# Kernel tuning notes

Measured on AMD Instinct MI355X. Metric: run time of the kernel, lower is better.

The kernel has to match this reference:

```python
import jax, jax.numpy as jnp
import numpy as np

B, C_IN, C_OUT, H, W = 16, 64, 64, 192, 192
K_DY, KS, STRIDE, PAD = 4, 3, 1, 1
TEMP = 30.0
HID = int(C_IN * 0.25) + 1  # 17, matches hidden_channels rule for in_channels != 3
GROUPS = 8
EPS = 1e-5
NEG_SLOPE = 0.01


def setup_inputs() -> dict:
    key = jax.random.key(0)
    ks = jax.random.split(key, 6)
    return {
        "x": jax.random.normal(ks[0], (B, C_IN, H, W), jnp.float32),
        "attn_w1": jax.random.normal(ks[1], (HID, C_IN), jnp.float32) * 0.1,   # 1x1 conv, no bias
        "attn_w2": jax.random.normal(ks[2], (K_DY, HID), jnp.float32) * 0.1,   # 1x1 conv
        "attn_b2": jnp.zeros((K_DY,), jnp.float32),
        "weights": jax.random.normal(ks[3], (K_DY, C_OUT, C_IN, KS, KS), jnp.float32),
        "gn_gamma": jnp.ones((C_OUT,), jnp.float32),
        "gn_beta": jnp.zeros((C_OUT,), jnp.float32),
    }


def reference(x, attn_w1, attn_w2, attn_b2, weights, gn_gamma, gn_beta):
    b = x.shape[0]
    # SE-style attention over the dynamic-filter bank
    pooled = x.mean(axis=(2, 3))                       # (b, c_in) global avg pool
    h = jax.nn.relu(pooled @ attn_w1.T)                # (b, hid)
    scores = h @ attn_w2.T + attn_b2                   # (b, K)
    attn = jax.nn.softmax(scores / TEMP, axis=1)       # (b, K)
    # Per-sample synthesized filters
    filters = jnp.einsum('bk,koihw->boihw', attn, weights)   # (b, out_c, in_c, kh, kw)
    filters = filters.reshape(b * C_OUT, C_IN, KS, KS)
    # Grouped conv: groups = batch, each sample convolved with its own filter
    xg = x.reshape(1, b * C_IN, H, W)
    y = jax.lax.conv_general_dilated(
        xg, filters,
        window_strides=(STRIDE, STRIDE),
        padding=[(PAD, PAD), (PAD, PAD)],
        dimension_numbers=('NCHW', 'OIHW', 'NCHW'),
        feature_group_count=b,
    )
    y = y.reshape(b, C_OUT, y.shape[2], y.shape[3])
    # GroupNorm(8 groups) + LeakyReLU
    yg = y.reshape(b, GROUPS, C_OUT // GROUPS, y.shape[2], y.shape[3])
    mean = yg.mean(axis=(2, 3, 4), keepdims=True)
    var = yg.var(axis=(2, 3, 4), keepdims=True)
    yn = ((yg - mean) * jax.lax.rsqrt(var + EPS)).reshape(y.shape)
    yn = yn * gn_gamma[None, :, None, None] + gn_beta[None, :, None, None]
    return jnp.where(yn >= 0, yn, NEG_SLOPE * yn)
```

## Files before the change

kernel.cpp:

```cpp
#include <hip/hip_runtime.h>

typedef unsigned short u16;
typedef unsigned int u32;
typedef _Float16 f16;
typedef __attribute__((ext_vector_type(8))) f16 v8h;
typedef __attribute__((ext_vector_type(4))) f16 v4h;
typedef __attribute__((ext_vector_type(16))) float v16f;

#define BN 16
#define CHN 64
#define HH 192
#define WW 192
#define HWSZ 36864
#define KDY 4
#define HIDN 17
#define NG 8
#define TEMP_ 30.0f
#define EPSV 1e-5f
#define NSLOPE 0.01f
#define NTILE 144

#define TR 8
#define TC 32
#define HR 10
#define HC 34
#define PSTR 34

__device__ float g_pp[BN * NTILE * CHN];
__device__ float g_attn[BN * KDY];
__device__ float g_stats[BN * NG * 2];
__device__ __align__(16) f16 g_filt[BN * 9 * CHN * CHN];
__device__ __align__(16) f16 g_xh[(size_t)BN * HWSZ * CHN];

__global__ void __launch_bounds__(256) trans_pool_kernel(const float* __restrict__ x) {
    __shared__ u32 ts[256 * 34];
    const int b = blockIdx.y, tile = blockIdx.x;
    const int t = threadIdx.x;
    const int p0 = tile * 256;
    const float* xb = x + (size_t)b * CHN * HWSZ + p0;
    #pragma unroll 4
    for (int cp = 0; cp < 32; cp++) {
        float v0 = xb[(size_t)(2 * cp) * HWSZ + t];
        float v1 = xb[(size_t)(2 * cp + 1) * HWSZ + t];
        u32 pk = (u32)__builtin_bit_cast(u16, (f16)v0)
               | ((u32)__builtin_bit_cast(u16, (f16)v1) << 16);
        ts[t * 34 + cp] = pk;
    }
    __syncthreads();
    f16* dp = g_xh + ((size_t)b * HWSZ + p0 + t) * CHN;
    const u32* src = ts + t * 34;
    #pragma unroll
    for (int i = 0; i < 8; i++) {
        uint2 a = *(const uint2*)(src + 4 * i);
        uint2 c = *(const uint2*)(src + 4 * i + 2);
        ((uint4*)dp)[i] = make_uint4(a.x, a.y, c.x, c.y);
    }
    const int cp = t & 31, seg = t >> 5;
    float s0 = 0.f, s1 = 0.f;
    for (int p = 0; p < 32; p++) {
        u32 pk = ts[(seg * 32 + p) * 34 + cp];
        s0 += (float)__builtin_bit_cast(f16, (u16)(pk & 0xffffu));
        s1 += (float)__builtin_bit_cast(f16, (u16)(pk >> 16));
    }
    s0 += __shfl_down(s0, 32);
    s1 += __shfl_down(s1, 32);
    __syncthreads();
    float* ps = (float*)ts;
    const int lane = t & 63, w = t >> 6;
    if (lane < 32) { ps[(w * 32 + lane) * 2] = s0; ps[(w * 32 + lane) * 2 + 1] = s1; }
    __syncthreads();
    if (t < 32) {
        float a0 = ps[t * 2] + ps[(32 + t) * 2] + ps[(64 + t) * 2] + ps[(96 + t) * 2];
        float a1 = ps[t * 2 + 1] + ps[(32 + t) * 2 + 1]
                 + ps[(64 + t) * 2 + 1] + ps[(96 + t) * 2 + 1];
        float* gp = g_pp + ((size_t)b * NTILE + tile) * CHN;
        gp[2 * t] = a0; gp[2 * t + 1] = a1;
    }
}

__global__ void attn_kernel(const float* __restrict__ w1, const float* __restrict__ w2,
                            const float* __restrict__ b2) {
    const int b = blockIdx.x, t = threadIdx.x;
    if (t < NG * 2) g_stats[b * NG * 2 + t] = 0.f;
    float s = 0.f;
    const float* gp = g_pp + (size_t)b * NTILE * CHN + t;
    for (int i = 0; i < NTILE; i++) s += gp[i * CHN];
    __shared__ float pr[CHN];
    __shared__ float hs[HIDN];
    pr[t] = s * (1.0f / HWSZ);
    __syncthreads();
    if (t < HIDN) {
        float a = 0.f;
        for (int c = 0; c < CHN; c++) a += w1[t * CHN + c] * pr[c];
        hs[t] = fmaxf(a, 0.f);
    }
    __syncthreads();
    if (t == 0) {
        float scv[KDY]; float m = -3e38f;
        #pragma unroll
        for (int k = 0; k < KDY; k++) {
            float sc = b2[k];
            for (int h = 0; h < HIDN; h++) sc += w2[k * HIDN + h] * hs[h];
            sc *= (1.0f / TEMP_);
            scv[k] = sc; m = fmaxf(m, sc);
        }
        float den = 0.f;
        #pragma unroll
        for (int k = 0; k < KDY; k++) { scv[k] = __expf(scv[k] - m); den += scv[k]; }
        float rd = 1.f / den;
        #pragma unroll
        for (int k = 0; k < KDY; k++) g_attn[b * KDY + k] = scv[k] * rd;
    }
}

__global__ void filt_kernel(const float* __restrict__ wts) {
    __shared__ float at[BN * KDY];
    if (threadIdx.x < BN * KDY) at[threadIdx.x] = g_attn[threadIdx.x];
    __syncthreads();
    int t = blockIdx.x * 256 + threadIdx.x;
    int tap = t / 4096;
    int co = (t >> 6) & 63;
    int ci = t & 63;
    float w0 = wts[((0 * CHN + co) * CHN + ci) * 9 + tap];
    float w1 = wts[((1 * CHN + co) * CHN + ci) * 9 + tap];
    float w2 = wts[((2 * CHN + co) * CHN + ci) * 9 + tap];
    float w3 = wts[((3 * CHN + co) * CHN + ci) * 9 + tap];
    #pragma unroll
    for (int b = 0; b < BN; b++) {
        float v = at[b * 4] * w0 + at[b * 4 + 1] * w1
                + at[b * 4 + 2] * w2 + at[b * 4 + 3] * w3;
        g_filt[((b * 9 + tap) * CHN + co) * CHN + ci] = (f16)v;
    }
}

__global__ void __launch_bounds__(256, 3) conv_kernel(float* __restrict__ y) {
    __shared__ __align__(16) u32 xs[HR * HC * PSTR];
    __shared__ float gsum[NG], gsq[NG];
    const int b = blockIdx.z;
    const int r0 = blockIdx.y * TR, c0 = blockIdx.x * TC;
    const int tid = threadIdx.x;
    const int w = tid >> 6, lane = tid & 63;
    const int n = lane & 31, hi = lane >> 5;
    if (tid < NG) { gsum[tid] = 0.f; gsq[tid] = 0.f; }

    const f16* xhb = g_xh + (size_t)b * HWSZ * CHN;
    for (int l = tid; l < HR * HC * 8; l += 256) {
        int pix = l >> 3, part = l & 7;
        int hr = pix / HC, hc = pix - hr * HC;
        int gr = r0 - 1 + hr, gc = c0 - 1 + hc;
        uint4 v = make_uint4(0, 0, 0, 0);
        if ((unsigned)gr < HH && (unsigned)gc < WW)
            v = *(const uint4*)(xhb + ((size_t)(gr * WW + gc)) * CHN + part * 8);
        u32* d = xs + pix * PSTR + part * 4;
        *(uint2*)d = make_uint2(v.x, v.y);
        *(uint2*)(d + 2) = make_uint2(v.z, v.w);
    }
    __syncthreads();

    const f16* xsh = (const f16*)xs;
    const f16* fb = g_filt + (size_t)b * 9 * CHN * CHN + (size_t)n * CHN + hi * 8;
    v16f acc00 = {}, acc01 = {}, acc10 = {}, acc11 = {};

    v8h A0[4], A1[4];
    #pragma unroll
    for (int kb = 0; kb < 4; kb++) {
        A0[kb] = *(const v8h*)(fb + kb * 16);
        A1[kb] = *(const v8h*)(fb + kb * 16 + 32 * CHN);
    }
    #pragma unroll
    for (int tap = 0; tap < 9; tap++) {
        v8h P0[4], P1[4];
        if (tap < 8) {
            const f16* fp = fb + (tap + 1) * (CHN * CHN);
            #pragma unroll
            for (int kb = 0; kb < 4; kb++) {
                P0[kb] = *(const v8h*)(fp + kb * 16);
                P1[kb] = *(const v8h*)(fp + kb * 16 + 32 * CHN);
            }
        }
        const int dy = tap / 3, dx = tap - 3 * (tap / 3);
        const f16* xr = xsh + ((2 * w + dy) * HC + (n + dx)) * (PSTR * 2) + hi * 8;
        #pragma unroll
        for (int kb = 0; kb < 4; kb++) {
            v4h lo0 = *(const v4h*)(xr + kb * 16);
            v4h up0 = *(const v4h*)(xr + kb * 16 + 4);
            v4h lo1 = *(const v4h*)(xr + kb * 16 + HC * PSTR * 2);
            v4h up1 = *(const v4h*)(xr + kb * 16 + 4 + HC * PSTR * 2);
            v8h b0 = __builtin_shufflevector(lo0, up0, 0, 1, 2, 3, 4, 5, 6, 7);
            v8h b1 = __builtin_shufflevector(lo1, up1, 0, 1, 2, 3, 4, 5, 6, 7);
            acc00 = __builtin_amdgcn_mfma_f32_32x32x16_f16(A0[kb], b0, acc00, 0, 0, 0);
            acc01 = __builtin_amdgcn_mfma_f32_32x32x16_f16(A0[kb], b1, acc01, 0, 0, 0);
            acc10 = __builtin_amdgcn_mfma_f32_32x32x16_f16(A1[kb], b0, acc10, 0, 0, 0);
            acc11 = __builtin_amdgcn_mfma_f32_32x32x16_f16(A1[kb], b1, acc11, 0, 0, 0);
        }
        if (tap < 8) {
            #pragma unroll
            for (int kb = 0; kb < 4; kb++) { A0[kb] = P0[kb]; A1[kb] = P1[kb]; }
        }
    }

    float sg[NG], sq[NG];
    #pragma unroll
    for (int g = 0; g < NG; g++) { sg[g] = 0.f; sq[g] = 0.f; }
    float* yb = y + (size_t)b * CHN * HWSZ + (size_t)(r0 + 2 * w) * WW + (c0 + n);
#define EPI(ACC, CH, J) { v16f a = ACC; \
    _Pragma("unroll") \
    for (int r = 0; r < 16; r++) { \
        int co = CH * 32 + (r & 3) + 8 * (r >> 2) + 4 * hi; \
        yb[(size_t)co * HWSZ + J * WW] = a[r]; \
        int g = (r >> 2) + 4 * CH; \
        sg[g] += a[r]; sq[g] += a[r] * a[r]; } }
    EPI(acc00, 0, 0) EPI(acc01, 0, 1) EPI(acc10, 1, 0) EPI(acc11, 1, 1)
#undef EPI
    #pragma unroll
    for (int g = 0; g < NG; g++) {
        float s = sg[g], q = sq[g];
        #pragma unroll
        for (int off = 32; off > 0; off >>= 1) {
            s += __shfl_down(s, off);
            q += __shfl_down(q, off);
        }
        if (lane == 0) { atomicAdd(&gsum[g], s); atomicAdd(&gsq[g], q); }
    }
    __syncthreads();
    if (tid < 2 * NG) {
        int g = tid >> 1, which = tid & 1;
        atomicAdd(&g_stats[(b * NG + g) * 2 + which], which ? gsq[g] : gsum[g]);
    }
}

__global__ void norm_kernel(float* __restrict__ y, const float* __restrict__ gamma,
                            const float* __restrict__ beta) {
    int i8 = blockIdx.x * 256 + threadIdx.x;
    int idx = i8 * 8;
    int b = idx / (CHN * HWSZ);
    int co = (idx / HWSZ) & (CHN - 1);
    int g = co >> 3;
    const float invN = 1.0f / (8.0f * HWSZ);
    float mean = g_stats[(b * NG + g) * 2 + 0] * invN;
    float var = fmaxf(g_stats[(b * NG + g) * 2 + 1] * invN - mean * mean, 0.f);
    float sc = rsqrtf(var + EPSV) * gamma[co];
    float sh = beta[co] - mean * sc;
    float4* yp = (float4*)y + i8 * 2;
    float4 v0 = yp[0], v1 = yp[1];
    float vv[8] = {v0.x, v0.y, v0.z, v0.w, v1.x, v1.y, v1.z, v1.w};
    #pragma unroll
    for (int t = 0; t < 8; t++) {
        float a = vv[t] * sc + sh;
        vv[t] = a >= 0.f ? a : NSLOPE * a;
    }
    yp[0] = make_float4(vv[0], vv[1], vv[2], vv[3]);
    yp[1] = make_float4(vv[4], vv[5], vv[6], vv[7]);
}

extern "C" void kernel_launch(void* const* d_in, const int* in_sizes, int n_in,
                              void* d_out, int out_size, void* d_ws, size_t ws_size,
                              hipStream_t stream) {
    const float* x     = (const float*)d_in[0];
    const float* w1    = (const float*)d_in[1];
    const float* w2    = (const float*)d_in[2];
    const float* b2    = (const float*)d_in[3];
    const float* wts   = (const float*)d_in[4];
    const float* gamma = (const float*)d_in[5];
    const float* beta  = (const float*)d_in[6];
    float* out = (float*)d_out;

    dim3 tg(NTILE, BN);
    trans_pool_kernel<<<tg, 256, 0, stream>>>(x);
    attn_kernel<<<BN, 64, 0, stream>>>(w1, w2, b2);
    filt_kernel<<<144, 256, 0, stream>>>(wts);
    dim3 cg(WW / TC, HH / TR, BN);
    conv_kernel<<<cg, 256, 0, stream>>>(out);
    norm_kernel<<<BN * CHN * HWSZ / 8 / 256, 256, 0, stream>>>(out, gamma, beta);
}
```

Before: 432.1 us.

## Store conv output as fp16 intermediate, batch halo loads, swizzle blocks, widen attn

The conv kernel now writes its pre-norm output to an fp16 scratch buffer, and the norm kernel reads that buffer before writing the fp32 output. This halves the intermediate write and read traffic, at some precision cost before GroupNorm. The halo load is split into issuing all global loads into registers first and then storing to LDS, which adds memory-level parallelism but uses more registers. Blocks are remapped with an XCD-style swizzle, and the attention pooling reduction now uses 256 threads instead of 64.

After: 406.7 us. 5.9% less time.

```diff
diff --git a/kernel.cpp b/kernel.cpp
--- a/kernel.cpp
+++ b/kernel.cpp
@@ -25,12 +25,14 @@
 #define HR 10
 #define HC 34
 #define PSTR 34
+#define NCHUNK (HR * HC * 8)
 
 __device__ float g_pp[BN * NTILE * CHN];
 __device__ float g_attn[BN * KDY];
 __device__ float g_stats[BN * NG * 2];
 __device__ __align__(16) f16 g_filt[BN * 9 * CHN * CHN];
 __device__ __align__(16) f16 g_xh[(size_t)BN * HWSZ * CHN];
+__device__ __align__(16) f16 g_yh[(size_t)BN * CHN * HWSZ];
 
 __global__ void __launch_bounds__(256) trans_pool_kernel(const float* __restrict__ x) {
     __shared__ u32 ts[256 * 34];
@@ -78,20 +80,27 @@
     }
 }
 
-__global__ void attn_kernel(const float* __restrict__ w1, const float* __restrict__ w2,
-                            const float* __restrict__ b2) {
+__global__ void __launch_bounds__(256) attn_kernel(const float* __restrict__ w1,
+                                                   const float* __restrict__ w2,
+                                                   const float* __restrict__ b2) {
+    __shared__ float red[256];
+    __shared__ float pr[CHN];
+    __shared__ float hs[HIDN];
     const int b = blockIdx.x, t = threadIdx.x;
     if (t < NG * 2) g_stats[b * NG * 2 + t] = 0.f;
+    const int c = t & 63, part = t >> 6;
+    const float* gp = g_pp + (size_t)b * NTILE * CHN + c;
     float s = 0.f;
-    const float* gp = g_pp + (size_t)b * NTILE * CHN + t;
-    for (int i = 0; i < NTILE; i++) s += gp[i * CHN];
-    __shared__ float pr[CHN];
-    __shared__ float hs[HIDN];
-    pr[t] = s * (1.0f / HWSZ);
+    #pragma unroll 4
+    for (int i = part * 36; i < part * 36 + 36; i++) s += gp[i * CHN];
+    red[t] = s;
+    __syncthreads();
+    if (t < CHN)
+        pr[t] = (red[t] + red[t + 64] + red[t + 128] + red[t + 192]) * (1.0f / HWSZ);
     __syncthreads();
     if (t < HIDN) {
         float a = 0.f;
-        for (int c = 0; c < CHN; c++) a += w1[t * CHN + c] * pr[c];
+        for (int cc = 0; cc < CHN; cc++) a += w1[t * CHN + cc] * pr[cc];
         hs[t] = fmaxf(a, 0.f);
     }
     __syncthreads();
@@ -133,27 +142,44 @@
     }
 }
 
-__global__ void __launch_bounds__(256, 3) conv_kernel(float* __restrict__ y) {
+__global__ void __launch_bounds__(256, 3) conv_kernel() {
     __shared__ __align__(16) u32 xs[HR * HC * PSTR];
     __shared__ float gsum[NG], gsq[NG];
-    const int b = blockIdx.z;
-    const int r0 = blockIdx.y * TR, c0 = blockIdx.x * TC;
+    const int bid = blockIdx.x;
+    const int swz = (bid & 7) * 288 + (bid >> 3);
+    const int b = swz / 144;
+    const int rem = swz - b * 144;
+    const int r0 = (rem / 6) * TR, c0 = (rem % 6) * TC;
     const int tid = threadIdx.x;
     const int w = tid >> 6, lane = tid & 63;
     const int n = lane & 31, hi = lane >> 5;
     if (tid < NG) { gsum[tid] = 0.f; gsq[tid] = 0.f; }
 
     const f16* xhb = g_xh + (size_t)b * HWSZ * CHN;
-    for (int l = tid; l < HR * HC * 8; l += 256) {
+    uint4 rv[11];
+    #pragma unroll
+    for (int i = 0; i < 11; i++) {
+        int l = tid + i * 256;
         int pix = l >> 3, part = l & 7;
         int hr = pix / HC, hc = pix - hr * HC;
         int gr = r0 - 1 + hr, gc = c0 - 1 + hc;
-        uint4 v = make_uint4(0, 0, 0, 0);
-        if ((unsigned)gr < HH && (unsigned)gc < WW)
-            v = *(const uint4*)(xhb + ((size_t)(gr * WW + gc)) * CHN + part * 8);
-        u32* d = xs + pix * PSTR + part * 4;
-        *(uint2*)d = make_uint2(v.x, v.y);
-        *(uint2*)(d + 2) = make_uint2(v.z, v.w);
+        bool ok = (l < NCHUNK) && ((unsigned)gr < HH) && ((unsigned)gc < WW);
+        size_t off = ok ? ((size_t)(gr * WW + gc) * CHN + part * 8) : 0;
+        rv[i] = *(const uint4*)(xhb + off);
+    }
+    #pragma unroll
+    for (int i = 0; i < 11; i++) {
+        int l = tid + i * 256;
+        if (l < NCHUNK) {
+            int pix = l >> 3, part = l & 7;
+            int hr = pix / HC, hc = pix - hr * HC;
+            int gr = r0 - 1 + hr, gc = c0 - 1 + hc;
+            bool ok = ((unsigned)gr < HH) && ((unsigned)gc < WW);
+            uint4 v = ok ? rv[i] : make_uint4(0, 0, 0, 0);
+            u32* d = xs + pix * PSTR + part * 4;
+            *(uint2*)d = make_uint2(v.x, v.y);
+            *(uint2*)(d + 2) = make_uint2(v.z, v.w);
+        }
     }
     __syncthreads();
 
@@ -202,12 +228,12 @@
     float sg[NG], sq[NG];
     #pragma unroll
     for (int g = 0; g < NG; g++) { sg[g] = 0.f; sq[g] = 0.f; }
-    float* yb = y + (size_t)b * CHN * HWSZ + (size_t)(r0 + 2 * w) * WW + (c0 + n);
+    f16* yb = g_yh + (size_t)b * CHN * HWSZ + (size_t)(r0 + 2 * w) * WW + (c0 + n);
 #define EPI(ACC, CH, J) { v16f a = ACC; \
     _Pragma("unroll") \
     for (int r = 0; r < 16; r++) { \
         int co = CH * 32 + (r & 3) + 8 * (r >> 2) + 4 * hi; \
-        yb[(size_t)co * HWSZ + J * WW] = a[r]; \
+        yb[(size_t)co * HWSZ + J * WW] = (f16)a[r]; \
         int g = (r >> 2) + 4 * CH; \
         sg[g] += a[r]; sq[g] += a[r] * a[r]; } }
     EPI(acc00, 0, 0) EPI(acc01, 0, 1) EPI(acc10, 1, 0) EPI(acc11, 1, 1)
@@ -229,7 +255,7 @@
     }
 }
 
-__global__ void norm_kernel(float* __restrict__ y, const float* __restrict__ gamma,
+__global__ void norm_kernel(float* __restrict__ out, const float* __restrict__ gamma,
                             const float* __restrict__ beta) {
     int i8 = blockIdx.x * 256 + threadIdx.x;
     int idx = i8 * 8;
@@ -241,16 +267,16 @@
     float var = fmaxf(g_stats[(b * NG + g) * 2 + 1] * invN - mean * mean, 0.f);
     float sc = rsqrtf(var + EPSV) * gamma[co];
     float sh = beta[co] - mean * sc;
-    float4* yp = (float4*)y + i8 * 2;
-    float4 v0 = yp[0], v1 = yp[1];
-    float vv[8] = {v0.x, v0.y, v0.z, v0.w, v1.x, v1.y, v1.z, v1.w};
+    v8h v = *(const v8h*)(g_yh + (size_t)idx);
+    float vv[8];
     #pragma unroll
     for (int t = 0; t < 8; t++) {
-        float a = vv[t] * sc + sh;
+        float a = (float)v[t] * sc + sh;
         vv[t] = a >= 0.f ? a : NSLOPE * a;
     }
-    yp[0] = make_float4(vv[0], vv[1], vv[2], vv[3]);
-    yp[1] = make_float4(vv[4], vv[5], vv[6], vv[7]);
+    float4* op = (float4*)out + i8 * 2;
+    op[0] = make_float4(vv[0], vv[1], vv[2], vv[3]);
+    op[1] = make_float4(vv[4], vv[5], vv[6], vv[7]);
 }
 
 extern "C" void kernel_launch(void* const* d_in, const int* in_sizes, int n_in,
@@ -267,9 +293,8 @@
 
     dim3 tg(NTILE, BN);
     trans_pool_kernel<<<tg, 256, 0, stream>>>(x);
-    attn_kernel<<<BN, 64, 0, stream>>>(w1, w2, b2);
+    attn_kernel<<<BN, 256, 0, stream>>>(w1, w2, b2);
     filt_kernel<<<144, 256, 0, stream>>>(wts);
-    dim3 cg(WW / TC, HH / TR, BN);
-    conv_kernel<<<cg, 256, 0, stream>>>(out);
+    conv_kernel<<<2304, 256, 0, stream>>>();
     norm_kernel<<<BN * CHN * HWSZ / 8 / 256, 256, 0, stream>>>(out, gamma, beta);
 }
```
